# Optimization experiments

Measured on AMD Instinct MI355X. Metric: run time of the kernel, lower is better.

## Reference

```python
import jax, jax.numpy as jnp
import numpy as np

B, C, D = 1024, 100000, 512
S_SCALE, MARGIN, EPS = 64.0, 0.5, 1e-7  # arcface defaults


def setup_inputs() -> dict:
    key = jax.random.key(0)
    kx, kl, kw = jax.random.split(key, 3)
    x = jax.random.normal(kx, (B, D), dtype=jnp.float32)
    labels = jax.random.randint(kl, (B,), 0, C, dtype=jnp.int64)
    # nn.Linear default init: U(-1/sqrt(fan_in), 1/sqrt(fan_in))
    bound = 1.0 / np.sqrt(D)
    W = jax.random.uniform(kw, (C, D), dtype=jnp.float32, minval=-bound, maxval=bound)
    return {"x": x, "labels": labels, "W": W}


def reference(x, labels, W):
    # L2-normalize features (W is NOT normalized in the original -- the
    # normalize loop there rebinds a local and is a no-op).
    xn = x / jnp.maximum(jnp.linalg.norm(x, axis=1, keepdims=True), 1e-12)
    wf = jnp.einsum('bd,cd->bc', xn, W)               # [B, C] cosine-like logits
    target = jnp.take_along_axis(wf, labels[:, None], axis=1)[:, 0]  # [B]
    # arcface: s * cos(acos(clamp(cos_theta)) + m)
    numerator = S_SCALE * jnp.cos(
        jnp.arccos(jnp.clip(target, -1.0 + EPS, 1.0 - EPS)) + MARGIN)
    # sum over excluded classes = full sum - label term
    excl_sum = jnp.sum(jnp.exp(S_SCALE * wf), axis=1) - jnp.exp(S_SCALE * target)
    L = numerator - jnp.log(jnp.exp(numerator) + excl_sum)
    return -jnp.mean(L)
```

## Files before the change

kernel.cpp:

```cpp
#include <hip/hip_runtime.h>
#include <hip/hip_bf16.h>
#include <math.h>

#define NB 1024
#define NC 100000
#define ND 512
#define SSCALE 64.0f
#define MMARGIN 0.5f

#define BM 128
#define BN 128
#define BK 64
#define NKS (ND / BK)
#define NRT (NB / BM)
#define NCT ((NC + BN - 1) / BN)
#define GRIDSZ (NRT * NCT)
#define NCPAD (NCT * BN)

#define ABUF  16384
#define BBASE 32768
#define BBUF  16384

typedef __bf16 bf16x8 __attribute__((ext_vector_type(8)));
typedef float f32x4 __attribute__((ext_vector_type(4)));

__device__ __forceinline__ void gload_lds16(const void* g, void* l) {
    __builtin_amdgcn_global_load_lds(
        (const __attribute__((address_space(1))) unsigned int*)g,
        (__attribute__((address_space(3))) unsigned int*)l, 16, 0, 0);
}


__global__ void prep_kernel(const float* __restrict__ x, __bf16* __restrict__ xnb) {
    const int row = blockIdx.x;
    const int tid = threadIdx.x;
    const float2 v = *reinterpret_cast<const float2*>(x + (size_t)row * ND + tid * 2);
    float ss = v.x * v.x + v.y * v.y;
#pragma unroll
    for (int m = 1; m < 64; m <<= 1) ss += __shfl_xor(ss, m);
    __shared__ float wsum[4];
    if ((tid & 63) == 0) wsum[tid >> 6] = ss;
    __syncthreads();
    const float tot = wsum[0] + wsum[1] + wsum[2] + wsum[3];
    const float inv = 1.0f / fmaxf(sqrtf(tot), 1e-12f);
    __bf16* dst = xnb + (size_t)row * ND + tid * 2;
    dst[0] = (__bf16)(v.x * inv);
    dst[1] = (__bf16)(v.y * inv);
}

__global__ void target_kernel(const __bf16* __restrict__ xnb, const float* __restrict__ Wg,
                              const int* __restrict__ labels, float* __restrict__ tgt) {
    const int wid  = threadIdx.x >> 6;
    const int lane = threadIdx.x & 63;
    const int row  = blockIdx.x * 4 + wid;
    const int lab  = labels[row];
    const int k    = lane * 8;
    const bf16x8 xv = *reinterpret_cast<const bf16x8*>(xnb + (size_t)row * ND + k);
    const float* wr = Wg + (size_t)lab * ND + k;
    const float4 w0 = *reinterpret_cast<const float4*>(wr);
    const float4 w1 = *reinterpret_cast<const float4*>(wr + 4);
    float s = (float)xv[0] * w0.x + (float)xv[1] * w0.y + (float)xv[2] * w0.z + (float)xv[3] * w0.w
            + (float)xv[4] * w1.x + (float)xv[5] * w1.y + (float)xv[6] * w1.z + (float)xv[7] * w1.w;
#pragma unroll
    for (int m = 1; m < 64; m <<= 1) s += __shfl_xor(s, m);
    if (lane == 0) tgt[row] = s;
}

__global__ void cvtw_kernel(const float* __restrict__ W, __bf16* __restrict__ Wbf) {
    const size_t gid = (size_t)blockIdx.x * 256 + threadIdx.x;
    bf16x8 h = {};
    if (gid * 8 < (size_t)NC * ND) {
        const float4 v0 = *reinterpret_cast<const float4*>(W + gid * 8);
        const float4 v1 = *reinterpret_cast<const float4*>(W + gid * 8 + 4);
        h[0] = (__bf16)v0.x; h[1] = (__bf16)v0.y; h[2] = (__bf16)v0.z; h[3] = (__bf16)v0.w;
        h[4] = (__bf16)v1.x; h[5] = (__bf16)v1.y; h[6] = (__bf16)v1.z; h[7] = (__bf16)v1.w;
    }
    *reinterpret_cast<bf16x8*>(Wbf + gid * 8) = h;
}

template<int BMODE>
__global__ __launch_bounds__(256, 2) void gemm_exp_kernel(const __bf16* __restrict__ xnb,
                                                          const void* __restrict__ Bsrc,
                                                          float* __restrict__ sums) {
    __shared__ char lds[65536];
    const int tid  = threadIdx.x;
    const int wid  = tid >> 6;
    const int lane = tid & 63;
    const int l15  = lane & 15;
    const int lhi  = lane >> 4;
    const int wr   = wid >> 1;
    const int wc   = wid & 1;

    const int logical = (blockIdx.x & 7) * (GRIDSZ / 8) + (blockIdx.x >> 3);
    const int rt = logical & 7;
    const int ct = logical >> 3;
    const int r0 = rt * BM;
    const int c0 = ct * BN;

    auto stageA = [&](int t, int buf) {
#pragma unroll
        for (int s = 0; s < 4; ++s) {
            const int row = s * 32 + wid * 8 + (lane >> 3);
            const int lc  = (lane & 7) ^ (row & 7);
            const char* src = (const char*)xnb + (size_t)(r0 + row) * 1024 + t * 128 + lc * 16;
            gload_lds16(src, lds + buf * ABUF + s * 4096 + wid * 1024);
        }
    };
    auto stageB = [&](int t, int buf) {
#pragma unroll
        for (int s = 0; s < 4; ++s) {
            const int cls = s * 32 + wid * 8 + (lane >> 3);
            const int lc  = (lane & 7) ^ (cls & 7);
            const char* src = (const char*)Bsrc + (size_t)(c0 + cls) * 1024 + t * 128 + lc * 16;
            gload_lds16(src, lds + BBASE + buf * BBUF + s * 4096 + wid * 1024);
        }
    };
    const int bcls = tid >> 3;
    const int bqp  = tid & 7;
    float4 bw[8];
    auto loadB = [&](int t) {
#pragma unroll
        for (int l = 0; l < 4; ++l) {
            const int cls = l * 32 + bcls;
            const float* src = (const float*)Bsrc + (size_t)(c0 + cls) * ND + t * BK + bqp * 8;
            if (c0 + cls < NC) {
                bw[l * 2]     = *reinterpret_cast<const float4*>(src);
                bw[l * 2 + 1] = *reinterpret_cast<const float4*>(src + 4);
            } else {
                bw[l * 2]     = make_float4(0.f, 0.f, 0.f, 0.f);
                bw[l * 2 + 1] = make_float4(0.f, 0.f, 0.f, 0.f);
            }
        }
    };
    auto writeB = [&](int buf) {
#pragma unroll
        for (int l = 0; l < 4; ++l) {
            const int cls = l * 32 + bcls;
            struct alignas(16) bf8s { __bf16 h[8]; };
            bf8s h;
            const float4 v0 = bw[l * 2], v1 = bw[l * 2 + 1];
            h.h[0] = (__bf16)v0.x; h.h[1] = (__bf16)v0.y; h.h[2] = (__bf16)v0.z; h.h[3] = (__bf16)v0.w;
            h.h[4] = (__bf16)v1.x; h.h[5] = (__bf16)v1.y; h.h[6] = (__bf16)v1.z; h.h[7] = (__bf16)v1.w;
            const int byte = BBASE + buf * BBUF + cls * 128 + ((bqp ^ (cls & 7)) << 4);
            *reinterpret_cast<bf8s*>(lds + byte) = h;
        }
    };

    f32x4 acc[4][4] = {};

    auto compute = [&](int buf) {
#pragma unroll
        for (int kk = 0; kk < 2; ++kk) {
            bf16x8 a[4], b[4];
            const int ck = (kk << 2) | lhi;
#pragma unroll
            for (int i = 0; i < 4; ++i) {
                const int r = wr * 64 + i * 16 + l15;
                a[i] = *reinterpret_cast<const bf16x8*>(
                    lds + buf * ABUF + r * 128 + ((ck ^ (r & 7)) << 4));
            }
#pragma unroll
            for (int j = 0; j < 4; ++j) {
                const int cls = wc * 64 + j * 16 + l15;
                b[j] = *reinterpret_cast<const bf16x8*>(
                    lds + BBASE + buf * BBUF + cls * 128 + ((ck ^ (cls & 7)) << 4));
            }
#pragma unroll
            for (int i = 0; i < 4; ++i)
#pragma unroll
                for (int j = 0; j < 4; ++j)
                    acc[i][j] = __builtin_amdgcn_mfma_f32_16x16x32_bf16(a[i], b[j], acc[i][j], 0, 0, 0);
        }
    };

    if constexpr (BMODE == 0) {
        stageA(0, 0);
        stageB(0, 0);
        __syncthreads();
#pragma unroll 1
        for (int t = 0; t < NKS; ++t) {
            const int buf = t & 1;
            if (t + 1 < NKS) {
                stageA(t + 1, buf ^ 1);
                stageB(t + 1, buf ^ 1);
            }
            compute(buf);
            __syncthreads();
        }
    } else {
        loadB(0);
        stageA(0, 0);
        loadB(1);
        writeB(0);
        __syncthreads();
#pragma unroll 1
        for (int t = 0; t < NKS; ++t) {
            const int buf = t & 1;
            if (t + 1 < NKS) {
                stageA(t + 1, buf ^ 1);
                loadB(t + 1);
            }
            compute(buf);
            if (t + 1 < NKS) writeB(buf ^ 1);
            __syncthreads();
        }
    }

#pragma unroll
    for (int i = 0; i < 4; ++i) {
#pragma unroll
        for (int r = 0; r < 4; ++r) {
            float v = 0.f;
#pragma unroll
            for (int j = 0; j < 4; ++j) {
                const int c = c0 + wc * 64 + j * 16 + l15;
                v += (c < NC) ? __expf(SSCALE * acc[i][j][r]) : 0.f;
            }
            v += __shfl_xor(v, 1);
            v += __shfl_xor(v, 2);
            v += __shfl_xor(v, 4);
            v += __shfl_xor(v, 8);
            if (l15 == 0) {
                const int row = r0 + wr * 64 + i * 16 + lhi * 4 + r;
                atomicAdd(&sums[row], v);
            }
        }
    }
}

__global__ void finalize_kernel(const float* __restrict__ sums, const float* __restrict__ tgt,
                                float* __restrict__ out) {
    const int tid  = threadIdx.x;
    const int wid  = tid >> 6;
    const int lane = tid & 63;
    float t  = tgt[tid];
    const float se = sums[tid];
    t = fminf(fmaxf(t, -1.0f + 1e-7f), 1.0f - 1e-7f);
    const float numer = SSCALE * cosf(acosf(t) + MMARGIN);
    const float excl  = se - expf(SSCALE * t);
    float L = numer - logf(expf(numer) + excl);
#pragma unroll
    for (int m = 1; m < 64; m <<= 1) L += __shfl_xor(L, m);
    __shared__ float ws2[16];
    if (lane == 0) ws2[wid] = L;
    __syncthreads();
    if (tid == 0) {
        float tot = 0.f;
        for (int i = 0; i < 16; ++i) tot += ws2[i];
        out[0] = -(tot / (float)NB);
    }
}

extern "C" void kernel_launch(void* const* d_in, const int* in_sizes, int n_in,
                              void* d_out, int out_size, void* d_ws, size_t ws_size,
                              hipStream_t stream) {
    const float* x      = (const float*)d_in[0];
    const int*   labels = (const int*)d_in[1];
    const float* W      = (const float*)d_in[2];
    float* out = (float*)d_out;

    char* wsb = (char*)d_ws;
    __bf16* xnb  = (__bf16*)wsb;
    float*  sums = (float*)(wsb + 1048576);
    float*  tgt  = (float*)(wsb + 1052672);
    __bf16* Wbf  = (__bf16*)(wsb + 1056768);
    const size_t WS_NEED = 1056768ull + (size_t)NCPAD * ND * 2;

    hipMemsetAsync(sums, 0, NB * sizeof(float), stream);
    prep_kernel<<<NB, 256, 0, stream>>>(x, xnb);
    target_kernel<<<NB / 4, 256, 0, stream>>>(xnb, W, labels, tgt);
    if (ws_size >= WS_NEED) {
        cvtw_kernel<<<((size_t)NCPAD * ND) / (256 * 8), 256, 0, stream>>>(W, Wbf);
        gemm_exp_kernel<0><<<GRIDSZ, 256, 0, stream>>>(xnb, Wbf, sums);
    } else {
        gemm_exp_kernel<1><<<GRIDSZ, 256, 0, stream>>>(xnb, W, sums);
    }
    finalize_kernel<<<1, 1024, 0, stream>>>(sums, tgt, out);
}
```

Measured before the change: 240.6 us.

## Enlarge GEMM tiles to 256x256 with 8 waves and interleaved prefetch schedule

Grows the fused GEMM+exp tile from 128x128 to 256x256, using 512 threads (8 waves), 128KB LDS, and a new swizzle layout. The K loop is split into four phases that interleave global-to-LDS prefetch with MFMA blocks, using explicit barriers and s_setprio. The aim is to raise arithmetic intensity and cut redundant global traffic for W and x. The trade-off is fewer workgroups (about 1564), higher register pressure from 32 accumulators per wave, and possible wave-quantization imbalance. The fp32 fallback path is kept as a separate kernel.

```diff
diff --git a/kernel.cpp b/kernel.cpp
--- a/kernel.cpp
+++ b/kernel.cpp
@@ -8,8 +8,8 @@
 #define SSCALE 64.0f
 #define MMARGIN 0.5f
 
-#define BM 128
-#define BN 128
+#define BM 256
+#define BN 256
 #define BK 64
 #define NKS (ND / BK)
 #define NRT (NB / BM)
@@ -17,9 +17,8 @@
 #define GRIDSZ (NRT * NCT)
 #define NCPAD (NCT * BN)
 
-#define ABUF  16384
-#define BBASE 32768
-#define BBUF  16384
+#define ABUF  32768
+#define BBASE 65536
 
 typedef __bf16 bf16x8 __attribute__((ext_vector_type(8)));
 typedef float f32x4 __attribute__((ext_vector_type(4)));
@@ -78,10 +77,148 @@
     *reinterpret_cast<bf16x8*>(Wbf + gid * 8) = h;
 }
 
-template<int BMODE>
-__global__ __launch_bounds__(256, 2) void gemm_exp_kernel(const __bf16* __restrict__ xnb,
-                                                          const void* __restrict__ Bsrc,
+__global__ __launch_bounds__(512, 2) void gemm_exp_kernel(const __bf16* __restrict__ xnb,
+                                                          const __bf16* __restrict__ Wbf,
                                                           float* __restrict__ sums) {
+    __shared__ char lds[131072];
+    const int tid  = threadIdx.x;
+    const int wid  = tid >> 6;
+    const int lane = tid & 63;
+    const int l15  = lane & 15;
+    const int lhi  = lane >> 4;
+    const int wr   = wid >> 2;
+    const int wc   = wid & 3;
+
+    const int xcd = blockIdx.x & 7, idx = blockIdx.x >> 3;
+    const int q = GRIDSZ >> 3, rr = GRIDSZ & 7;
+    const int wgid = (xcd < rr ? xcd * (q + 1) : rr * (q + 1) + (xcd - rr) * q) + idx;
+    const int rt = wgid & 3;
+    const int ct = wgid >> 2;
+    const int r0 = rt * BM;
+    const int c0 = ct * BN;
+
+    int aoff[2][4], boff[4];
+#pragma unroll
+    for (int ih = 0; ih < 2; ++ih)
+#pragma unroll
+        for (int i = 0; i < 4; ++i) {
+            const int r = wr * 128 + (ih * 4 + i) * 16 + l15;
+            aoff[ih][i] = r * 128 + ((lhi ^ (r & 3)) << 4) + (((r >> 2) & 1) << 6);
+        }
+#pragma unroll
+    for (int j = 0; j < 4; ++j) {
+        const int cls = wc * 64 + j * 16 + l15;
+        boff[j] = cls * 128 + ((lhi ^ (cls & 3)) << 4) + (((cls >> 2) & 1) << 6);
+    }
+    size_t aoffg[4], boffg[4];
+#pragma unroll
+    for (int s = 0; s < 4; ++s) {
+        const int lin = s * 8192 + wid * 1024 + lane * 16;
+        const int row = lin >> 7;
+        const int ck  = (lin >> 4) & 7;
+        const int sw  = (ck ^ (row & 7)) << 4;
+        aoffg[s] = (size_t)(r0 + row) * 1024 + sw;
+        boffg[s] = (size_t)(c0 + row) * 1024 + sw;
+    }
+
+    auto stA = [&](int t, int nb, int s) {
+        gload_lds16((const char*)xnb + aoffg[s] + (size_t)t * 128,
+                    lds + nb * ABUF + s * 8192 + wid * 1024);
+    };
+    auto stB = [&](int t, int nb, int s) {
+        gload_lds16((const char*)Wbf + boffg[s] + (size_t)t * 128,
+                    lds + BBASE + nb * ABUF + s * 8192 + wid * 1024);
+    };
+    auto readA = [&](int ab, const int (&ao)[4], int kk, bf16x8 (&a)[4]) {
+#pragma unroll
+        for (int i = 0; i < 4; ++i)
+            a[i] = *reinterpret_cast<const bf16x8*>(lds + ab + (ao[i] ^ (kk << 6)));
+    };
+    auto readB = [&](int bb, int kk, bf16x8 (&b)[4]) {
+#pragma unroll
+        for (int j = 0; j < 4; ++j)
+            b[j] = *reinterpret_cast<const bf16x8*>(lds + bb + (boff[j] ^ (kk << 6)));
+    };
+
+    f32x4 acc[8][4] = {};
+
+#define MFMA16(AC, A, B)                                                      \
+    _Pragma("unroll")                                                         \
+    for (int i = 0; i < 4; ++i)                                               \
+        _Pragma("unroll")                                                     \
+        for (int j = 0; j < 4; ++j)                                           \
+            (AC)[i][j] = __builtin_amdgcn_mfma_f32_16x16x32_bf16(             \
+                (A)[i], (B)[j], (AC)[i][j], 0, 0, 0);
+
+#define SYNC_PRE                                                              \
+    __builtin_amdgcn_s_barrier();                                             \
+    asm volatile("s_waitcnt lgkmcnt(0)" ::: "memory");                        \
+    __builtin_amdgcn_sched_barrier(0);                                        \
+    __builtin_amdgcn_s_setprio(1);
+
+#define SYNC_POST                                                             \
+    __builtin_amdgcn_s_setprio(0);                                            \
+    __builtin_amdgcn_s_barrier();
+
+#pragma unroll
+    for (int s = 0; s < 4; ++s) { stA(0, 0, s); stB(0, 0, s); }
+    asm volatile("s_waitcnt vmcnt(0) lgkmcnt(0)\ns_barrier" ::: "memory");
+
+#pragma unroll 1
+    for (int kt = 0; kt < NKS; ++kt) {
+        const int cur = kt & 1, nxt = cur ^ 1;
+        const int ab = cur * ABUF, bb = BBASE + cur * ABUF;
+        const bool pf = (kt + 1) < NKS;
+        bf16x8 afr[4], bfr[4];
+
+        readB(bb, 0, bfr);
+        readA(ab, aoff[0], 0, afr);
+        if (pf) { stA(kt + 1, nxt, 0); stA(kt + 1, nxt, 1); }
+        SYNC_PRE; MFMA16(&acc[0], afr, bfr); SYNC_POST;
+
+        readA(ab, aoff[1], 0, afr);
+        if (pf) { stA(kt + 1, nxt, 2); stA(kt + 1, nxt, 3); stB(kt + 1, nxt, 0); }
+        SYNC_PRE; MFMA16(&acc[4], afr, bfr); SYNC_POST;
+
+        readB(bb, 1, bfr);
+        readA(ab, aoff[0], 1, afr);
+        if (pf) { stB(kt + 1, nxt, 1); stB(kt + 1, nxt, 2); stB(kt + 1, nxt, 3); }
+        SYNC_PRE; MFMA16(&acc[0], afr, bfr); SYNC_POST;
+
+        readA(ab, aoff[1], 1, afr);
+        SYNC_PRE; MFMA16(&acc[4], afr, bfr);
+        __builtin_amdgcn_s_setprio(0);
+        asm volatile("s_waitcnt vmcnt(0) lgkmcnt(0)\ns_barrier" ::: "memory");
+    }
+
+#pragma unroll
+    for (int i = 0; i < 8; ++i) {
+#pragma unroll
+        for (int r = 0; r < 4; ++r) {
+            float v = 0.f;
+#pragma unroll
+            for (int j = 0; j < 4; ++j) {
+                const int c = c0 + wc * 64 + j * 16 + l15;
+                v += (c < NC) ? __expf(SSCALE * acc[i][j][r]) : 0.f;
+            }
+            v += __shfl_xor(v, 1);
+            v += __shfl_xor(v, 2);
+            v += __shfl_xor(v, 4);
+            v += __shfl_xor(v, 8);
+            if (l15 == 0) {
+                const int row = r0 + wr * 128 + i * 16 + lhi * 4 + r;
+                atomicAdd(&sums[row], v);
+            }
+        }
+    }
+#undef MFMA16
+#undef SYNC_PRE
+#undef SYNC_POST
+}
+
+__global__ __launch_bounds__(256, 2) void gemm_exp_fb(const __bf16* __restrict__ xnb,
+                                                      const float* __restrict__ Wg,
+                                                      float* __restrict__ sums) {
     __shared__ char lds[65536];
     const int tid  = threadIdx.x;
     const int wid  = tid >> 6;
@@ -90,31 +227,9 @@
     const int lhi  = lane >> 4;
     const int wr   = wid >> 1;
     const int wc   = wid & 1;
-
-    const int logical = (blockIdx.x & 7) * (GRIDSZ / 8) + (blockIdx.x >> 3);
-    const int rt = logical & 7;
-    const int ct = logical >> 3;
-    const int r0 = rt * BM;
-    const int c0 = ct * BN;
-
-    auto stageA = [&](int t, int buf) {
-#pragma unroll
-        for (int s = 0; s < 4; ++s) {
-            const int row = s * 32 + wid * 8 + (lane >> 3);
-            const int lc  = (lane & 7) ^ (row & 7);
-            const char* src = (const char*)xnb + (size_t)(r0 + row) * 1024 + t * 128 + lc * 16;
-            gload_lds16(src, lds + buf * ABUF + s * 4096 + wid * 1024);
-        }
-    };
-    auto stageB = [&](int t, int buf) {
-#pragma unroll
-        for (int s = 0; s < 4; ++s) {
-            const int cls = s * 32 + wid * 8 + (lane >> 3);
-            const int lc  = (lane & 7) ^ (cls & 7);
-            const char* src = (const char*)Bsrc + (size_t)(c0 + cls) * 1024 + t * 128 + lc * 16;
-            gload_lds16(src, lds + BBASE + buf * BBUF + s * 4096 + wid * 1024);
-        }
-    };
+    const int logical = (blockIdx.x & 7) * (6256 / 8) + (blockIdx.x >> 3);
+    const int r0 = (logical & 7) * 128;
+    const int c0 = (logical >> 3) * 128;
     const int bcls = tid >> 3;
     const int bqp  = tid & 7;
     float4 bw[8];
@@ -122,13 +237,13 @@
 #pragma unroll
         for (int l = 0; l < 4; ++l) {
             const int cls = l * 32 + bcls;
-            const float* src = (const float*)Bsrc + (size_t)(c0 + cls) * ND + t * BK + bqp * 8;
+            const float* src = Wg + (size_t)(c0 + cls) * ND + t * 64 + bqp * 8;
             if (c0 + cls < NC) {
                 bw[l * 2]     = *reinterpret_cast<const float4*>(src);
                 bw[l * 2 + 1] = *reinterpret_cast<const float4*>(src + 4);
             } else {
-                bw[l * 2]     = make_float4(0.f, 0.f, 0.f, 0.f);
-                bw[l * 2 + 1] = make_float4(0.f, 0.f, 0.f, 0.f);
+                bw[l * 2] = make_float4(0.f, 0.f, 0.f, 0.f);
+                bw[l * 2 + 1] = bw[l * 2];
             }
         }
     };
@@ -141,13 +256,20 @@
             const float4 v0 = bw[l * 2], v1 = bw[l * 2 + 1];
             h.h[0] = (__bf16)v0.x; h.h[1] = (__bf16)v0.y; h.h[2] = (__bf16)v0.z; h.h[3] = (__bf16)v0.w;
             h.h[4] = (__bf16)v1.x; h.h[5] = (__bf16)v1.y; h.h[6] = (__bf16)v1.z; h.h[7] = (__bf16)v1.w;
-            const int byte = BBASE + buf * BBUF + cls * 128 + ((bqp ^ (cls & 7)) << 4);
-            *reinterpret_cast<bf8s*>(lds + byte) = h;
-        }
-    };
-
+            *reinterpret_cast<bf8s*>(lds + 32768 + buf * 16384 + cls * 128 +
+                                     ((bqp ^ (cls & 7)) << 4)) = h;
+        }
+    };
+    auto stageA = [&](int t, int buf) {
+#pragma unroll
+        for (int s = 0; s < 4; ++s) {
+            const int row = s * 32 + wid * 8 + (lane >> 3);
+            const int lc  = (lane & 7) ^ (row & 7);
+            gload_lds16((const char*)xnb + (size_t)(r0 + row) * 1024 + t * 128 + lc * 16,
+                        lds + buf * 16384 + s * 4096 + wid * 1024);
+        }
+    };
     f32x4 acc[4][4] = {};
-
     auto compute = [&](int buf) {
 #pragma unroll
         for (int kk = 0; kk < 2; ++kk) {
@@ -156,14 +278,12 @@
 #pragma unroll
             for (int i = 0; i < 4; ++i) {
                 const int r = wr * 64 + i * 16 + l15;
-                a[i] = *reinterpret_cast<const bf16x8*>(
-                    lds + buf * ABUF + r * 128 + ((ck ^ (r & 7)) << 4));
+                a[i] = *reinterpret_cast<const bf16x8*>(lds + buf * 16384 + r * 128 + ((ck ^ (r & 7)) << 4));
             }
 #pragma unroll
             for (int j = 0; j < 4; ++j) {
                 const int cls = wc * 64 + j * 16 + l15;
-                b[j] = *reinterpret_cast<const bf16x8*>(
-                    lds + BBASE + buf * BBUF + cls * 128 + ((ck ^ (cls & 7)) << 4));
+                b[j] = *reinterpret_cast<const bf16x8*>(lds + 32768 + buf * 16384 + cls * 128 + ((ck ^ (cls & 7)) << 4));
             }
 #pragma unroll
             for (int i = 0; i < 4; ++i)
@@ -172,40 +292,18 @@
                     acc[i][j] = __builtin_amdgcn_mfma_f32_16x16x32_bf16(a[i], b[j], acc[i][j], 0, 0, 0);
         }
     };
-
-    if constexpr (BMODE == 0) {
-        stageA(0, 0);
-        stageB(0, 0);
+    loadB(0);
+    stageA(0, 0);
+    writeB(0);
+    __syncthreads();
+#pragma unroll 1
+    for (int t = 0; t < 8; ++t) {
+        const int buf = t & 1;
+        if (t + 1 < 8) { stageA(t + 1, buf ^ 1); loadB(t + 1); }
+        compute(buf);
+        if (t + 1 < 8) writeB(buf ^ 1);
         __syncthreads();
-#pragma unroll 1
-        for (int t = 0; t < NKS; ++t) {
-            const int buf = t & 1;
-            if (t + 1 < NKS) {
-                stageA(t + 1, buf ^ 1);
-                stageB(t + 1, buf ^ 1);
-            }
-            compute(buf);
-            __syncthreads();
-        }
-    } else {
-        loadB(0);
-        stageA(0, 0);
-        loadB(1);
-        writeB(0);
-        __syncthreads();
-#pragma unroll 1
-        for (int t = 0; t < NKS; ++t) {
-            const int buf = t & 1;
-            if (t + 1 < NKS) {
-                stageA(t + 1, buf ^ 1);
-                loadB(t + 1);
-            }
-            compute(buf);
-            if (t + 1 < NKS) writeB(buf ^ 1);
-            __syncthreads();
-        }
-    }
-
+    }
 #pragma unroll
     for (int i = 0; i < 4; ++i) {
 #pragma unroll
@@ -220,10 +318,7 @@
             v += __shfl_xor(v, 2);
             v += __shfl_xor(v, 4);
             v += __shfl_xor(v, 8);
-            if (l15 == 0) {
-                const int row = r0 + wr * 64 + i * 16 + lhi * 4 + r;
-                atomicAdd(&sums[row], v);
-            }
+            if (l15 == 0) atomicAdd(&sums[r0 + wr * 64 + i * 16 + lhi * 4 + r], v);
         }
     }
 }
@@ -271,9 +366,9 @@
     target_kernel<<<NB / 4, 256, 0, stream>>>(xnb, W, labels, tgt);
     if (ws_size >= WS_NEED) {
         cvtw_kernel<<<((size_t)NCPAD * ND) / (256 * 8), 256, 0, stream>>>(W, Wbf);
-        gemm_exp_kernel<0><<<GRIDSZ, 256, 0, stream>>>(xnb, Wbf, sums);
+        gemm_exp_kernel<<<GRIDSZ, 512, 0, stream>>>(xnb, Wbf, sums);
     } else {
-        gemm_exp_kernel<1><<<GRIDSZ, 256, 0, stream>>>(xnb, W, sums);
+        gemm_exp_fb<<<6256, 256, 0, stream>>>(xnb, W, sums);
     }
     finalize_kernel<<<1, 1024, 0, stream>>>(sums, tgt, out);
 }
```

Result: slower. 270.6 us (+12.5%).
